# Kernel tuning notes

Measured on AMD Instinct MI355X. Metric: run time of the kernel, lower is better.

Reference implementation:

```python
import jax, jax.numpy as jnp
import numpy as np

COMMITMENT_COST = 0.25

def setup_inputs() -> dict:
    key = jax.random.key(0)
    k1, k2 = jax.random.split(key)
    inputs = jax.random.normal(k1, (16, 256, 64, 64), dtype=jnp.float32)   # [B, C=D, H, W]
    embedding = jax.random.normal(k2, (2048, 256), dtype=jnp.float32)      # [K, D] codebook
    return {"inputs": inputs, "embedding": embedding}

def reference(inputs, embedding):
    K, D = embedding.shape
    x = jnp.transpose(inputs, (0, 2, 3, 1))            # [B, H, W, D]
    flat = x.reshape(-1, D)                            # [N, D]
    distances = (jnp.sum(flat * flat, axis=1, keepdims=True)
                 + jnp.sum(embedding * embedding, axis=1)
                 - 2.0 * flat @ embedding.T)
    idx = jnp.argmin(distances, axis=1)                # [N]
    encodings = jax.nn.one_hot(idx, K, dtype=flat.dtype)  # [N, K]
    quantized = embedding[idx].reshape(x.shape)        # gather == one_hot @ embedding
    # commitment loss (eval mode: only e_latent term, scaled)
    e_latent_loss = jnp.mean((jax.lax.stop_gradient(quantized) - x) ** 2)
    loss = COMMITMENT_COST * e_latent_loss
    # straight-through estimator
    quantized_st = x + jax.lax.stop_gradient(quantized - x)
    avg_probs = jnp.mean(encodings, axis=0)
    perplexity = jnp.exp(-jnp.sum(avg_probs * jnp.log(avg_probs + 1e-10)))
    return (loss,
            jnp.transpose(quantized_st, (0, 3, 1, 2)),  # back to [B, C, H, W]
            perplexity,
            encodings)
```

## Files before the change

### kernel.cpp

```cpp
#include <hip/hip_runtime.h>

#define NROWS   65536
#define KCODES  2048
#define DDIM    256
#define HWSZ    4096

#define OUT_LOSS 0
#define OUT_Q    1
#define OUT_PERP 16777217
#define OUT_ENC  16777218

#define SCR0     (OUT_ENC + 2)
#define SCR_XHI  (SCR0)
#define SCR_EHI  (SCR0 + 8388608)

#define WS_CAND 0
#define WS_E2   1048576
#define WS_CNT  1056768
#define WS_SUM  1064960

typedef _Float16 f16x8 __attribute__((ext_vector_type(8)));
typedef _Float16 f16x4 __attribute__((ext_vector_type(4)));
typedef float    f32x4 __attribute__((ext_vector_type(4)));

__device__ __forceinline__ void gld16(const void* g, void* l) {
    __builtin_amdgcn_global_load_lds((const __attribute__((address_space(1))) void*)g,
                                     (__attribute__((address_space(3))) void*)l, 16, 0, 0);
}

__launch_bounds__(256)
__global__ void k_split(const float* __restrict__ inp, _Float16* __restrict__ Xhi) {
    __shared__ float tile[32][33];
    const int hw0 = blockIdx.x * 32, d0 = blockIdx.y * 32, b = blockIdx.z;
    const int tx = threadIdx.x & 31, ty = threadIdx.x >> 5;
#pragma unroll
    for (int i = 0; i < 32; i += 8)
        tile[ty + i][tx] = inp[b * 1048576 + (d0 + ty + i) * 4096 + hw0 + tx];
    __syncthreads();
#pragma unroll
    for (int i = 0; i < 32; i += 8) {
        const int n = b * 4096 + hw0 + ty + i;
        Xhi[n * DDIM + d0 + tx] = (_Float16)tile[tx][ty + i];
    }
}

__launch_bounds__(256)
__global__ void k_e2split(const float* __restrict__ emb, _Float16* __restrict__ Ehi,
                          float* __restrict__ e2, int* __restrict__ counts,
                          float* __restrict__ sumsq) {
    const int wave = threadIdx.x >> 6;
    const int lane = threadIdx.x & 63;
    const int k = blockIdx.x * 4 + wave;
    const float4 v = *(const float4*)(emb + k * DDIM + lane * 4);
    f16x4 h;
    h[0] = (_Float16)v.x; h[1] = (_Float16)v.y; h[2] = (_Float16)v.z; h[3] = (_Float16)v.w;
    *(f16x4*)(Ehi + k * DDIM + lane * 4) = h;
    float s = v.x * v.x + v.y * v.y + v.z * v.z + v.w * v.w;
#pragma unroll
    for (int off = 32; off >= 1; off >>= 1) s += __shfl_down(s, off);
    if (lane == 0) e2[k] = s;
    if (blockIdx.x < 8) counts[blockIdx.x * 256 + threadIdx.x] = 0;
    if (blockIdx.x == 8 && threadIdx.x == 0) sumsq[0] = 0.0f;
}

#define MERGE2(m1,i1,m2,i2,n1,j1,n2,j2)                                   \
    {                                                                     \
        const bool w_ = ((n1) < (m1)) || ((n1) == (m1) && (j1) < (i1));   \
        const float w1_ = w_ ? (n1) : (m1); const int wi_ = w_ ? (j1) : (i1); \
        const float l1_ = w_ ? (m1) : (n1); const int li_ = w_ ? (i1) : (j1); \
        const float c2_ = w_ ? (n2) : (m2); const int ci_ = w_ ? (j2) : (i2); \
        const bool s_ = ((c2_) < (l1_)) || ((c2_) == (l1_) && (ci_) < (li_)); \
        (m1) = w1_; (i1) = wi_;                                           \
        (m2) = s_ ? c2_ : l1_; (i2) = s_ ? ci_ : li_;                     \
    }

__launch_bounds__(256, 2)
__global__ void k_topk(const _Float16* __restrict__ Xhi, const _Float16* __restrict__ Ehi,
                       const float* __restrict__ e2, int4* __restrict__ cand) {
    __shared__ _Float16 Ah[128 * 64];
    __shared__ _Float16 Bh[128 * 64];

    const int rb = blockIdx.x;
    const int n0 = rb * 128;
    const int tid = threadIdx.x;
    const int w = tid >> 6, lane = tid & 63;
    const int wr = (w >> 1) * 64, wc = (w & 1) * 64;
    const int lq = lane >> 4, lm = lane & 15;
    const int r = lane >> 3, c = lane & 7;
    const int gch = c ^ r;

    float V1[4][4], V2[4][4]; int I1[4][4], I2[4][4];
#pragma unroll
    for (int i = 0; i < 4; ++i)
#pragma unroll
        for (int rr = 0; rr < 4; ++rr) {
            V1[i][rr] = 3.402823466e38f; V2[i][rr] = 3.402823466e38f;
            I1[i][rr] = 0x7fffffff;      I2[i][rr] = 0x7fffffff;
        }

#pragma unroll 1
    for (int ct = 0; ct < 16; ++ct) {
        const int c0 = ct * 128;
        f32x4 acc[4][4];
#pragma unroll
        for (int i = 0; i < 4; ++i)
#pragma unroll
            for (int j = 0; j < 4; ++j) acc[i][j] = (f32x4)(0.0f);

#pragma unroll 1
        for (int kt = 0; kt < 4; ++kt) {
            const int d0 = kt * 64;
            __syncthreads();
#pragma unroll
            for (int i = 0; i < 4; ++i) {
                const int Row = i * 32 + w * 8 + r;
                gld16(Xhi + (size_t)(n0 + Row) * DDIM + d0 + gch * 8, &Ah[(i * 32 + w * 8) * 64]);
                gld16(Ehi + (size_t)(c0 + Row) * DDIM + d0 + gch * 8, &Bh[(i * 32 + w * 8) * 64]);
            }
            __syncthreads();
#pragma unroll
            for (int s = 0; s < 2; ++s) {
                const int wch = s * 4 + lq;
                f16x8 af[4], bf[4];
#pragma unroll
                for (int t = 0; t < 4; ++t) {
                    const int Ra = wr + t * 16 + lm;
                    const int Rb = wc + t * 16 + lm;
                    af[t] = *(const f16x8*)&Ah[Ra * 64 + ((wch ^ (Ra & 7)) * 8)];
                    bf[t] = *(const f16x8*)&Bh[Rb * 64 + ((wch ^ (Rb & 7)) * 8)];
                }
#pragma unroll
                for (int i = 0; i < 4; ++i)
#pragma unroll
                    for (int j = 0; j < 4; ++j)
                        acc[i][j] = __builtin_amdgcn_mfma_f32_16x16x32_f16(af[i], bf[j], acc[i][j], 0, 0, 0);
            }
        }

        float e2v[4];
#pragma unroll
        for (int j = 0; j < 4; ++j) e2v[j] = e2[c0 + wc + j * 16 + lm];
#pragma unroll
        for (int i = 0; i < 4; ++i)
#pragma unroll
            for (int j = 0; j < 4; ++j) {
                const int idx = c0 + wc + j * 16 + lm;
#pragma unroll
                for (int rr = 0; rr < 4; ++rr) {
                    const float dist = fmaf(-2.0f, acc[i][j][rr], e2v[j]);
                    const bool b1 = dist < V1[i][rr];
                    const bool b2 = dist < V2[i][rr];
                    V2[i][rr] = b1 ? V1[i][rr] : (b2 ? dist : V2[i][rr]);
                    I2[i][rr] = b1 ? I1[i][rr] : (b2 ? idx  : I2[i][rr]);
                    V1[i][rr] = b1 ? dist : V1[i][rr];
                    I1[i][rr] = b1 ? idx  : I1[i][rr];
                }
            }
    }

    __syncthreads();
    float4* red = (float4*)Ah;
#pragma unroll
    for (int i = 0; i < 4; ++i)
#pragma unroll
        for (int rr = 0; rr < 4; ++rr) {
            float m1 = V1[i][rr]; int i1 = I1[i][rr];
            float m2 = V2[i][rr]; int i2 = I2[i][rr];
#pragma unroll
            for (int off = 1; off < 16; off <<= 1) {
                const float n1 = __shfl_xor(m1, off); const int j1 = __shfl_xor(i1, off);
                const float n2 = __shfl_xor(m2, off); const int j2 = __shfl_xor(i2, off);
                MERGE2(m1, i1, m2, i2, n1, j1, n2, j2);
            }
            if (lm == 0) {
                const int row = wr + i * 16 + lq * 4 + rr;
                red[row * 2 + (w & 1)] = make_float4(m1, __int_as_float(i1),
                                                     m2, __int_as_float(i2));
            }
        }
    __syncthreads();
    if (tid < 128) {
        const float4 A = red[tid * 2];
        const float4 B = red[tid * 2 + 1];
        cand[n0 + tid] = make_int4(__float_as_int(A.y), __float_as_int(A.w),
                                   __float_as_int(B.y), __float_as_int(B.w));
    }
}

__launch_bounds__(256)
__global__ void k_tail(const float* __restrict__ inp, const float* __restrict__ emb,
                       const float* __restrict__ e2, const int4* __restrict__ cand,
                       int* __restrict__ counts, float* __restrict__ sumsq,
                       float* __restrict__ outQ, float2* __restrict__ enc) {
    __shared__ float part[4][64][5];
    __shared__ int   idxs[64];

    const int blk = blockIdx.x;
    const int b   = blk >> 6;
    const int hw0 = (blk & 63) << 6;
    const int w = threadIdx.x >> 6, lane = threadIdx.x & 63;
    const int n0 = (b << 12) + hw0;

    const int4 c4 = cand[n0 + lane];
    const float* xp  = inp + (size_t)b * 1048576 + (size_t)(w * 64) * 4096 + hw0 + lane;
    const float* ep0 = emb + (size_t)c4.x * DDIM + w * 64;
    const float* ep1 = emb + (size_t)c4.y * DDIM + w * 64;
    const float* ep2 = emb + (size_t)c4.z * DDIM + w * 64;
    const float* ep3 = emb + (size_t)c4.w * DDIM + w * 64;
    float s0 = 0.f, s1 = 0.f, s2 = 0.f, s3 = 0.f, x2 = 0.f;
#pragma unroll 8
    for (int dd = 0; dd < 64; ++dd) {
        const float xv = xp[(size_t)dd * 4096];
        s0 = fmaf(xv, ep0[dd], s0);
        s1 = fmaf(xv, ep1[dd], s1);
        s2 = fmaf(xv, ep2[dd], s2);
        s3 = fmaf(xv, ep3[dd], s3);
        x2 = fmaf(xv, xv, x2);
    }
    part[w][lane][0] = s0; part[w][lane][1] = s1; part[w][lane][2] = s2;
    part[w][lane][3] = s3; part[w][lane][4] = x2;
    __syncthreads();

    if (threadIdx.x < 64) {
        const int rr = threadIdx.x;
        float S[5];
#pragma unroll
        for (int k = 0; k < 5; ++k)
            S[k] = part[0][rr][k] + part[1][rr][k] + part[2][rr][k] + part[3][rr][k];
        const int4 cc = cand[n0 + rr];
        const int cid[4] = {cc.x, cc.y, cc.z, cc.w};
        float bv = 3.402823466e38f; int bi = 0; float sb = 0.f, eb = 0.f;
#pragma unroll
        for (int k = 0; k < 4; ++k) {
            const float ev = e2[cid[k]];
            const float dv = fmaf(-2.0f, S[k], ev);
            if (dv < bv || (dv == bv && cid[k] < bi)) { bv = dv; bi = cid[k]; sb = S[k]; eb = ev; }
        }
        idxs[rr] = bi;
        atomicAdd(&counts[bi], 1);
        float lr = S[4] - 2.0f * sb + eb;
#pragma unroll
        for (int off = 32; off >= 1; off >>= 1) lr += __shfl_down(lr, off);
        if (rr == 0) atomicAdd(sumsq, lr);
    }
    __syncthreads();

    const int myidx = idxs[lane];
    const float* qp = emb + (size_t)myidx * DDIM + w * 64;
    float* op = outQ + (size_t)b * 1048576 + (size_t)(w * 64) * 4096 + hw0 + lane;
#pragma unroll 8
    for (int dd = 0; dd < 64; ++dd) op[(size_t)dd * 4096] = qp[dd];

    float2* erow = enc + (size_t)n0 * 1024;
#pragma unroll 1
    for (int rr = 0; rr < 64; ++rr) {
        const int id = idxs[rr];
        float2* rp = erow + (size_t)rr * 1024;
#pragma unroll
        for (int k = 0; k < 4; ++k) {
            const int c2 = k * 256 + threadIdx.x;
            const int ccc = c2 * 2;
            float2 v;
            v.x = (ccc == id) ? 1.0f : 0.0f;
            v.y = (ccc + 1 == id) ? 1.0f : 0.0f;
            rp[c2] = v;
        }
    }
}

__launch_bounds__(256)
__global__ void k_finalize(const int* __restrict__ counts, const float* __restrict__ sumsq,
                           float* __restrict__ out) {
    __shared__ float red[256];
    const int t = threadIdx.x;
    float s = 0.0f;
    for (int k = t; k < KCODES; k += 256) {
        const float p = (float)counts[k] * (1.0f / 65536.0f);
        s += p * logf(p + 1e-10f);
    }
    red[t] = s;
    __syncthreads();
    for (int off = 128; off >= 1; off >>= 1) {
        if (t < off) red[t] += red[t + off];
        __syncthreads();
    }
    if (t == 0) {
        out[OUT_PERP] = expf(-red[0]);
        out[OUT_LOSS] = 0.25f * sumsq[0] * (1.0f / 16777216.0f);
    }
}

extern "C" void kernel_launch(void* const* d_in, const int* in_sizes, int n_in,
                              void* d_out, int out_size, void* d_ws, size_t ws_size,
                              hipStream_t stream) {
    const float* inp = (const float*)d_in[0];
    const float* emb = (const float*)d_in[1];
    float* out = (float*)d_out;
    char* wsb  = (char*)d_ws;

    _Float16* Xhi    = (_Float16*)(out + SCR_XHI);
    _Float16* Ehi    = (_Float16*)(out + SCR_EHI);
    int4*     cand   = (int4*)(wsb + WS_CAND);
    float*    e2     = (float*)(wsb + WS_E2);
    int*      counts = (int*)(wsb + WS_CNT);
    float*    sumsq  = (float*)(wsb + WS_SUM);

    k_split   <<<dim3(128, 8, 16), 256, 0, stream>>>(inp, Xhi);
    k_e2split <<<512,              256, 0, stream>>>(emb, Ehi, e2, counts, sumsq);
    k_topk    <<<512,              256, 0, stream>>>(Xhi, Ehi, e2, cand);
    k_tail    <<<1024,             256, 0, stream>>>(inp, emb, e2, cand, counts, sumsq,
                                                     out + OUT_Q, (float2*)(out + OUT_ENC));
    k_finalize<<<1,                256, 0, stream>>>(counts, sumsq, out);
}
```

Before: 887.2 us.

## Fuse input transpose, top-k GEMM and exact rescoring into one main kernel

```diff
diff --git a/kernel.cpp b/kernel.cpp
--- a/kernel.cpp
+++ b/kernel.cpp
@@ -1,48 +1,34 @@
 #include <hip/hip_runtime.h>
 
-#define NROWS   65536
 #define KCODES  2048
 #define DDIM    256
-#define HWSZ    4096
 
 #define OUT_LOSS 0
 #define OUT_Q    1
 #define OUT_PERP 16777217
 #define OUT_ENC  16777218
 
-#define SCR0     (OUT_ENC + 2)
-#define SCR_XHI  (SCR0)
-#define SCR_EHI  (SCR0 + 8388608)
-
-#define WS_CAND 0
+#define WS_IDX  0
 #define WS_E2   1048576
 #define WS_CNT  1056768
 #define WS_SUM  1064960
+#define WS_EHI  2097152
 
 typedef _Float16 f16x8 __attribute__((ext_vector_type(8)));
 typedef _Float16 f16x4 __attribute__((ext_vector_type(4)));
 typedef float    f32x4 __attribute__((ext_vector_type(4)));
-
-__device__ __forceinline__ void gld16(const void* g, void* l) {
-    __builtin_amdgcn_global_load_lds((const __attribute__((address_space(1))) void*)g,
-                                     (__attribute__((address_space(3))) void*)l, 16, 0, 0);
-}
-
-__launch_bounds__(256)
-__global__ void k_split(const float* __restrict__ inp, _Float16* __restrict__ Xhi) {
-    __shared__ float tile[32][33];
-    const int hw0 = blockIdx.x * 32, d0 = blockIdx.y * 32, b = blockIdx.z;
-    const int tx = threadIdx.x & 31, ty = threadIdx.x >> 5;
-#pragma unroll
-    for (int i = 0; i < 32; i += 8)
-        tile[ty + i][tx] = inp[b * 1048576 + (d0 + ty + i) * 4096 + hw0 + tx];
-    __syncthreads();
-#pragma unroll
-    for (int i = 0; i < 32; i += 8) {
-        const int n = b * 4096 + hw0 + ty + i;
-        Xhi[n * DDIM + d0 + tx] = (_Float16)tile[tx][ty + i];
-    }
-}
+typedef float    f32x2 __attribute__((ext_vector_type(2)));
+
+#define MERGE2(m1,i1,m2,i2,n1,j1,n2,j2)                                   \
+    {                                                                     \
+        const bool w_ = ((n1) < (m1)) || ((n1) == (m1) && (j1) < (i1));   \
+        const float w1_ = w_ ? (n1) : (m1); const int wi_ = w_ ? (j1) : (i1); \
+        const float l1_ = w_ ? (m1) : (n1); const int li_ = w_ ? (i1) : (j1); \
+        const float c2_ = w_ ? (n2) : (m2); const int ci_ = w_ ? (j2) : (i2); \
+        const bool s_ = ((c2_) < (l1_)) || ((c2_) == (l1_) && (ci_) < (li_)); \
+        (m1) = w1_; (i1) = wi_;                                           \
+        (m2) = s_ ? c2_ : l1_; (i2) = s_ ? ci_ : li_;                     \
+    }
 
 __launch_bounds__(256)
 __global__ void k_e2split(const float* __restrict__ emb, _Float16* __restrict__ Ehi,
@@ -63,31 +49,57 @@
     if (blockIdx.x == 8 && threadIdx.x == 0) sumsq[0] = 0.0f;
 }
 
-#define MERGE2(m1,i1,m2,i2,n1,j1,n2,j2)                                   \
-    {                                                                     \
-        const bool w_ = ((n1) < (m1)) || ((n1) == (m1) && (j1) < (i1));   \
-        const float w1_ = w_ ? (n1) : (m1); const int wi_ = w_ ? (j1) : (i1); \
-        const float l1_ = w_ ? (m1) : (n1); const int li_ = w_ ? (i1) : (j1); \
-        const float c2_ = w_ ? (n2) : (m2); const int ci_ = w_ ? (j2) : (i2); \
-        const bool s_ = ((c2_) < (l1_)) || ((c2_) == (l1_) && (ci_) < (li_)); \
-        (m1) = w1_; (i1) = wi_;                                           \
-        (m2) = s_ ? c2_ : l1_; (i2) = s_ ? ci_ : li_;                     \
-    }
-
 __launch_bounds__(256, 2)
-__global__ void k_topk(const _Float16* __restrict__ Xhi, const _Float16* __restrict__ Ehi,
-                       const float* __restrict__ e2, int4* __restrict__ cand) {
-    __shared__ _Float16 Ah[128 * 64];
-    __shared__ _Float16 Bh[128 * 64];
-
-    const int rb = blockIdx.x;
-    const int n0 = rb * 128;
+__global__ void k_main(const float* __restrict__ inp, const float* __restrict__ emb,
+                       const _Float16* __restrict__ Ehi, const float* __restrict__ e2g,
+                       int* __restrict__ idx_g, int* __restrict__ counts,
+                       float* __restrict__ sumsq) {
+    __shared__ __align__(16) _Float16 A[128 * 256];
+    __shared__ float e2s[KCODES];
+    __shared__ float xpart[4][128];
+
+    const int rb  = blockIdx.x;
+    const int b   = rb >> 5;
+    const int hw0 = (rb & 31) << 7;
+    const int n0  = rb << 7;
     const int tid = threadIdx.x;
     const int w = tid >> 6, lane = tid & 63;
+    const int lq = lane >> 4, lm = lane & 15;
     const int wr = (w >> 1) * 64, wc = (w & 1) * 64;
-    const int lq = lane >> 4, lm = lane & 15;
-    const int r = lane >> 3, c = lane & 7;
-    const int gch = c ^ r;
+
+    {
+        const float4* s = (const float4*)e2g;
+        float4* d = (float4*)e2s;
+        d[tid] = s[tid];
+        d[tid + 256] = s[tid + 256];
+    }
+
+    const float* base = inp + (size_t)b * 1048576 + hw0;
+    float x2lo = 0.f, x2hi = 0.f;
+#pragma unroll 4
+    for (int rr = 0; rr < 16; ++rr) {
+        const int row = ((rr & 1) << 6) + lane;
+        const int cg  = ((rr >> 1) << 2) + w;
+        const float* p = base + (size_t)(cg << 3) * 4096 + row;
+        float v[8];
+#pragma unroll
+        for (int j = 0; j < 8; ++j) v[j] = p[(size_t)j * 4096];
+        f16x8 h;
+        float s = 0.f;
+#pragma unroll
+        for (int j = 0; j < 8; ++j) { h[j] = (_Float16)v[j]; s = fmaf(v[j], v[j], s); }
+        if (rr & 1) x2hi += s; else x2lo += s;
+        const int q  = cg >> 3;
+        const int ch = cg & 7;
+        *(f16x8*)&A[row * 256 + q * 64 + ((ch ^ (row & 7)) << 3)] = h;
+    }
+    xpart[w][lane] = x2lo;
+    xpart[w][64 + lane] = x2hi;
+    __syncthreads();
+
+    const _Float16* Bb = Ehi + (size_t)(wc + lm) * 256 + lq * 8;
+    const int sw0 = ((lq    ) ^ (lm & 7)) << 3;
+    const int sw1 = ((lq ^ 4) ^ (lm & 7)) << 3;
 
     float V1[4][4], V2[4][4]; int I1[4][4], I2[4][4];
 #pragma unroll
@@ -107,39 +119,38 @@
 #pragma unroll
             for (int j = 0; j < 4; ++j) acc[i][j] = (f32x4)(0.0f);
 
-#pragma unroll 1
-        for (int kt = 0; kt < 4; ++kt) {
-            const int d0 = kt * 64;
-            __syncthreads();
-#pragma unroll
-            for (int i = 0; i < 4; ++i) {
-                const int Row = i * 32 + w * 8 + r;
-                gld16(Xhi + (size_t)(n0 + Row) * DDIM + d0 + gch * 8, &Ah[(i * 32 + w * 8) * 64]);
-                gld16(Ehi + (size_t)(c0 + Row) * DDIM + d0 + gch * 8, &Bh[(i * 32 + w * 8) * 64]);
+        f16x8 bn[4];
+#pragma unroll
+        for (int t = 0; t < 4; ++t)
+            bn[t] = *(const f16x8*)(Bb + (size_t)(c0 + t * 16) * 256);
+
+#pragma unroll
+        for (int g = 0; g < 8; ++g) {
+            f16x8 bf[4];
+#pragma unroll
+            for (int t = 0; t < 4; ++t) bf[t] = bn[t];
+            if (g < 7) {
+                const int dof = (((g + 1) >> 1) << 6) + (((g + 1) & 1) << 5);
+#pragma unroll
+                for (int t = 0; t < 4; ++t)
+                    bn[t] = *(const f16x8*)(Bb + (size_t)(c0 + t * 16) * 256 + dof);
             }
-            __syncthreads();
-#pragma unroll
-            for (int s = 0; s < 2; ++s) {
-                const int wch = s * 4 + lq;
-                f16x8 af[4], bf[4];
-#pragma unroll
-                for (int t = 0; t < 4; ++t) {
-                    const int Ra = wr + t * 16 + lm;
-                    const int Rb = wc + t * 16 + lm;
-                    af[t] = *(const f16x8*)&Ah[Ra * 64 + ((wch ^ (Ra & 7)) * 8)];
-                    bf[t] = *(const f16x8*)&Bh[Rb * 64 + ((wch ^ (Rb & 7)) * 8)];
-                }
-#pragma unroll
-                for (int i = 0; i < 4; ++i)
-#pragma unroll
-                    for (int j = 0; j < 4; ++j)
-                        acc[i][j] = __builtin_amdgcn_mfma_f32_16x16x32_f16(af[i], bf[j], acc[i][j], 0, 0, 0);
-            }
+            const int kt = g >> 1;
+            const int sw = (g & 1) ? sw1 : sw0;
+            f16x8 af[4];
+#pragma unroll
+            for (int t = 0; t < 4; ++t)
+                af[t] = *(const f16x8*)&A[(wr + t * 16 + lm) * 256 + kt * 64 + sw];
+#pragma unroll
+            for (int i = 0; i < 4; ++i)
+#pragma unroll
+                for (int j = 0; j < 4; ++j)
+                    acc[i][j] = __builtin_amdgcn_mfma_f32_16x16x32_f16(af[i], bf[j], acc[i][j], 0, 0, 0);
         }
 
         float e2v[4];
 #pragma unroll
-        for (int j = 0; j < 4; ++j) e2v[j] = e2[c0 + wc + j * 16 + lm];
+        for (int j = 0; j < 4; ++j) e2v[j] = e2s[c0 + wc + j * 16 + lm];
 #pragma unroll
         for (int i = 0; i < 4; ++i)
 #pragma unroll
@@ -159,7 +170,8 @@
     }
 
     __syncthreads();
-    float4* red = (float4*)Ah;
+    float4* red  = (float4*)&A[0];
+    float*  refp = (float*)&A[4096];
 #pragma unroll
     for (int i = 0; i < 4; ++i)
 #pragma unroll
@@ -179,91 +191,94 @@
             }
         }
     __syncthreads();
+
+    {
+        const int rg = w & 1, dh = w >> 1;
+        const int r  = (rg << 6) + lane;
+        const float4 Ac = red[r * 2];
+        const float4 Bc = red[r * 2 + 1];
+        const int c0i = __float_as_int(Ac.y), c1i = __float_as_int(Ac.w);
+        const int c2i = __float_as_int(Bc.y), c3i = __float_as_int(Bc.w);
+        const float* xp = base + (size_t)(dh * 128) * 4096 + r;
+        const float* p0 = emb + (size_t)c0i * DDIM + dh * 128;
+        const float* p1 = emb + (size_t)c1i * DDIM + dh * 128;
+        const float* p2 = emb + (size_t)c2i * DDIM + dh * 128;
+        const float* p3 = emb + (size_t)c3i * DDIM + dh * 128;
+        float s0 = 0.f, s1 = 0.f, s2 = 0.f, s3 = 0.f;
+#pragma unroll 8
+        for (int dd = 0; dd < 128; ++dd) {
+            const float xv = xp[(size_t)dd * 4096];
+            s0 = fmaf(xv, p0[dd], s0);
+            s1 = fmaf(xv, p1[dd], s1);
+            s2 = fmaf(xv, p2[dd], s2);
+            s3 = fmaf(xv, p3[dd], s3);
+        }
+        f32x4 sv; sv[0] = s0; sv[1] = s1; sv[2] = s2; sv[3] = s3;
+        *(f32x4*)&refp[(w * 64 + lane) * 4] = sv;
+    }
+    __syncthreads();
+
     if (tid < 128) {
-        const float4 A = red[tid * 2];
-        const float4 B = red[tid * 2 + 1];
-        cand[n0 + tid] = make_int4(__float_as_int(A.y), __float_as_int(A.w),
-                                   __float_as_int(B.y), __float_as_int(B.w));
+        const int r = tid;
+        const int g = r >> 6, rl = r & 63;
+        float S[4];
+#pragma unroll
+        for (int k = 0; k < 4; ++k)
+            S[k] = refp[(g * 64 + rl) * 4 + k] + refp[((g + 2) * 64 + rl) * 4 + k];
+        const float4 Ac = red[r * 2];
+        const float4 Bc = red[r * 2 + 1];
+        const int cid[4] = {__float_as_int(Ac.y), __float_as_int(Ac.w),
+                            __float_as_int(Bc.y), __float_as_int(Bc.w)};
+        float bv = 3.402823466e38f; int bi = 0; float sb = 0.f, eb = 0.f;
+#pragma unroll
+        for (int k = 0; k < 4; ++k) {
+            const float ev = e2s[cid[k]];
+            const float dv = fmaf(-2.0f, S[k], ev);
+            if (dv < bv || (dv == bv && cid[k] < bi)) { bv = dv; bi = cid[k]; sb = S[k]; eb = ev; }
+        }
+        idx_g[n0 + r] = bi;
+        atomicAdd(&counts[bi], 1);
+        const float x2r = xpart[0][r] + xpart[1][r] + xpart[2][r] + xpart[3][r];
+        float lr = x2r - 2.0f * sb + eb;
+#pragma unroll
+        for (int off = 32; off >= 1; off >>= 1) lr += __shfl_down(lr, off);
+        if ((r & 63) == 0) atomicAdd(sumsq, lr);
     }
 }
 
 __launch_bounds__(256)
-__global__ void k_tail(const float* __restrict__ inp, const float* __restrict__ emb,
-                       const float* __restrict__ e2, const int4* __restrict__ cand,
-                       int* __restrict__ counts, float* __restrict__ sumsq,
-                       float* __restrict__ outQ, float2* __restrict__ enc) {
-    __shared__ float part[4][64][5];
-    __shared__ int   idxs[64];
-
+__global__ void k_out(const float* __restrict__ emb, const int* __restrict__ idx_g,
+                      float* __restrict__ outQ, float* __restrict__ enc) {
+    __shared__ int idxs[64];
     const int blk = blockIdx.x;
     const int b   = blk >> 6;
     const int hw0 = (blk & 63) << 6;
     const int w = threadIdx.x >> 6, lane = threadIdx.x & 63;
     const int n0 = (b << 12) + hw0;
 
-    const int4 c4 = cand[n0 + lane];
-    const float* xp  = inp + (size_t)b * 1048576 + (size_t)(w * 64) * 4096 + hw0 + lane;
-    const float* ep0 = emb + (size_t)c4.x * DDIM + w * 64;
-    const float* ep1 = emb + (size_t)c4.y * DDIM + w * 64;
-    const float* ep2 = emb + (size_t)c4.z * DDIM + w * 64;
-    const float* ep3 = emb + (size_t)c4.w * DDIM + w * 64;
-    float s0 = 0.f, s1 = 0.f, s2 = 0.f, s3 = 0.f, x2 = 0.f;
-#pragma unroll 8
-    for (int dd = 0; dd < 64; ++dd) {
-        const float xv = xp[(size_t)dd * 4096];
-        s0 = fmaf(xv, ep0[dd], s0);
-        s1 = fmaf(xv, ep1[dd], s1);
-        s2 = fmaf(xv, ep2[dd], s2);
-        s3 = fmaf(xv, ep3[dd], s3);
-        x2 = fmaf(xv, xv, x2);
-    }
-    part[w][lane][0] = s0; part[w][lane][1] = s1; part[w][lane][2] = s2;
-    part[w][lane][3] = s3; part[w][lane][4] = x2;
-    __syncthreads();
-
-    if (threadIdx.x < 64) {
-        const int rr = threadIdx.x;
-        float S[5];
-#pragma unroll
-        for (int k = 0; k < 5; ++k)
-            S[k] = part[0][rr][k] + part[1][rr][k] + part[2][rr][k] + part[3][rr][k];
-        const int4 cc = cand[n0 + rr];
-        const int cid[4] = {cc.x, cc.y, cc.z, cc.w};
-        float bv = 3.402823466e38f; int bi = 0; float sb = 0.f, eb = 0.f;
-#pragma unroll
-        for (int k = 0; k < 4; ++k) {
-            const float ev = e2[cid[k]];
-            const float dv = fmaf(-2.0f, S[k], ev);
-            if (dv < bv || (dv == bv && cid[k] < bi)) { bv = dv; bi = cid[k]; sb = S[k]; eb = ev; }
-        }
-        idxs[rr] = bi;
-        atomicAdd(&counts[bi], 1);
-        float lr = S[4] - 2.0f * sb + eb;
-#pragma unroll
-        for (int off = 32; off >= 1; off >>= 1) lr += __shfl_down(lr, off);
-        if (rr == 0) atomicAdd(sumsq, lr);
-    }
+    if (threadIdx.x < 64) idxs[threadIdx.x] = idx_g[n0 + threadIdx.x];
     __syncthreads();
 
     const int myidx = idxs[lane];
     const float* qp = emb + (size_t)myidx * DDIM + w * 64;
     float* op = outQ + (size_t)b * 1048576 + (size_t)(w * 64) * 4096 + hw0 + lane;
 #pragma unroll 8
-    for (int dd = 0; dd < 64; ++dd) op[(size_t)dd * 4096] = qp[dd];
-
-    float2* erow = enc + (size_t)n0 * 1024;
+    for (int dd = 0; dd < 64; ++dd)
+        __builtin_nontemporal_store(qp[dd], op + (size_t)dd * 4096);
+
+    f32x2* erow = (f32x2*)enc + (size_t)n0 * 1024;
 #pragma unroll 1
     for (int rr = 0; rr < 64; ++rr) {
         const int id = idxs[rr];
-        float2* rp = erow + (size_t)rr * 1024;
+        f32x2* rp = erow + (size_t)rr * 1024;
 #pragma unroll
         for (int k = 0; k < 4; ++k) {
             const int c2 = k * 256 + threadIdx.x;
             const int ccc = c2 * 2;
-            float2 v;
-            v.x = (ccc == id) ? 1.0f : 0.0f;
-            v.y = (ccc + 1 == id) ? 1.0f : 0.0f;
-            rp[c2] = v;
+            f32x2 v;
+            v[0] = (ccc == id) ? 1.0f : 0.0f;
+            v[1] = (ccc + 1 == id) ? 1.0f : 0.0f;
+            __builtin_nontemporal_store(v, rp + c2);
         }
     }
 }
@@ -298,17 +313,14 @@
     float* out = (float*)d_out;
     char* wsb  = (char*)d_ws;
 
-    _Float16* Xhi    = (_Float16*)(out + SCR_XHI);
-    _Float16* Ehi    = (_Float16*)(out + SCR_EHI);
-    int4*     cand   = (int4*)(wsb + WS_CAND);
+    int*      idxg   = (int*)(wsb + WS_IDX);
     float*    e2     = (float*)(wsb + WS_E2);
     int*      counts = (int*)(wsb + WS_CNT);
     float*    sumsq  = (float*)(wsb + WS_SUM);
-
-    k_split   <<<dim3(128, 8, 16), 256, 0, stream>>>(inp, Xhi);
-    k_e2split <<<512,              256, 0, stream>>>(emb, Ehi, e2, counts, sumsq);
-    k_topk    <<<512,              256, 0, stream>>>(Xhi, Ehi, e2, cand);
-    k_tail    <<<1024,             256, 0, stream>>>(inp, emb, e2, cand, counts, sumsq,
-                                                     out + OUT_Q, (float2*)(out + OUT_ENC));
-    k_finalize<<<1,                256, 0, stream>>>(counts, sumsq, out);
-}
+    _Float16* Ehi    = (_Float16*)(wsb + WS_EHI);
+
+    k_e2split <<<512,  256, 0, stream>>>(emb, Ehi, e2, counts, sumsq);
+    k_main    <<<512,  256, 0, stream>>>(inp, emb, Ehi, e2, idxg, counts, sumsq);
+    k_out     <<<1024, 256, 0, stream>>>(emb, idxg, out + OUT_Q, out + OUT_ENC);
+    k_finalize<<<1,    256, 0, stream>>>(counts, sumsq, out);
+}
```

Result: slower. 977.6 us (+10.2%).
